# Kernel tuning notes

Hardware: AMD Instinct MI355X
Metric: run time of the kernel (lower is better)

Reference implementation:

```python
import jax, jax.numpy as jnp
import numpy as np

LAMBDA_GEO = 0.5


def setup_inputs() -> dict:
    key = jax.random.key(0)
    embeddings = jax.random.normal(key, (4, 2048, 512), dtype=jnp.float32)
    return {"embeddings": embeddings}


def _geometric_loss(embeddings):
    b, s, d = embeddings.shape
    x = embeddings.reshape(b * s, d)  # [N, d]
    sq_norm = jnp.sum(x * x, axis=-1)  # [N]
    sq = sq_norm[:, None] + sq_norm[None, :] - 2.0 * (x @ x.T)  # [N, N]
    sq = jnp.maximum(sq, 0.0)
    dist = jnp.sqrt(sq)  # torch.cdist(p=2)
    return jnp.mean(jnp.exp(-dist * 0.1)) * 0.1


def reference(embeddings):
    geometric_loss = _geometric_loss(embeddings)
    total_geometric = LAMBDA_GEO * geometric_loss
    return geometric_loss, total_geometric
```

## Files before the change

kernel.cpp:

```cpp
#include <hip/hip_runtime.h>

#define NROWS 8192
#define DIM   512
#define NT    64
#define NTRI  (NT * (NT + 1) / 2)
#define NACC  64

typedef __attribute__((ext_vector_type(16))) float f32x16;
typedef __attribute__((ext_vector_type(8)))  int   i32x8;

__device__ __forceinline__ unsigned char f2e4m3(float x) {
    unsigned ux = __float_as_uint(x);
    unsigned s  = (ux >> 24) & 0x80u;
    float a = __uint_as_float(ux & 0x7FFFFFFFu);
    a = fminf(a, 448.0f);
    unsigned ua = __float_as_uint(a);
    int eb = (int)(ua >> 23);
    if (eb < 121) eb = 121;
    float step  = __uint_as_float((unsigned)(eb - 3) << 23);
    float istep = __uint_as_float((unsigned)(257 - eb) << 23);
    float q = rintf(a * istep) * step;
    q = fminf(q, 448.0f);
    if (q < 0.001953125f)
        return (unsigned char)s;
    unsigned uq = __float_as_uint(q);
    int eq = (int)(uq >> 23) - 127;
    unsigned byte;
    if (eq < -6) byte = (unsigned)(q * 512.0f);
    else         byte = (unsigned)((eq + 7) << 3) | ((uq >> 20) & 7u);
    return (unsigned char)(s | byte);
}

__global__ __launch_bounds__(256) void norm_convert_kernel(
    const float* __restrict__ X, unsigned char* __restrict__ Xq,
    float* __restrict__ norms, float* __restrict__ acc)
{
    const int tid  = threadIdx.x;
    const int lane = tid & 63;
    const int w    = tid >> 6;
    const int row  = blockIdx.x * 4 + w;

    if (blockIdx.x == 0 && tid < NACC + 1) acc[tid] = 0.0f;

    const float* xr = X + (size_t)row * DIM + lane * 8;
    float4 v0 = *(const float4*)xr;
    float4 v1 = *(const float4*)(xr + 4);

    float s = 0.0f;
    s = fmaf(v0.x, v0.x, s); s = fmaf(v0.y, v0.y, s);
    s = fmaf(v0.z, v0.z, s); s = fmaf(v0.w, v0.w, s);
    s = fmaf(v1.x, v1.x, s); s = fmaf(v1.y, v1.y, s);
    s = fmaf(v1.z, v1.z, s); s = fmaf(v1.w, v1.w, s);

    union { unsigned char b[8]; uint2 v; } pk;
    pk.b[0] = f2e4m3(v0.x); pk.b[1] = f2e4m3(v0.y);
    pk.b[2] = f2e4m3(v0.z); pk.b[3] = f2e4m3(v0.w);
    pk.b[4] = f2e4m3(v1.x); pk.b[5] = f2e4m3(v1.y);
    pk.b[6] = f2e4m3(v1.z); pk.b[7] = f2e4m3(v1.w);

    const int slab = lane >> 3;
    const int c16  = (lane >> 1) & 3;
    const int cpos = c16 ^ ((row >> 1) & 3);
    *(uint2*)(Xq + (size_t)row * DIM + slab * 64 + cpos * 16 + (lane & 1) * 8)
        = pk.v;

    #pragma unroll
    for (int off = 32; off > 0; off >>= 1) s += __shfl_down(s, off, 64);
    if (lane == 0) norms[row] = s;
}

__device__ __forceinline__ void gload16(const void* g, void* l) {
    __builtin_amdgcn_global_load_lds(
        (const __attribute__((address_space(1))) unsigned int*)g,
        (__attribute__((address_space(3))) unsigned int*)l, 16, 0, 0);
}

__global__ __launch_bounds__(256, 3) void pair_loss_gemm_kernel(
    const unsigned char* __restrict__ Xq, const float* __restrict__ norms,
    float* __restrict__ acc, float* __restrict__ out)
{
    __shared__ __align__(16) char Ls[3][16384];
    __shared__ float wsum[4];
    __shared__ int lastflag;

    const int bid = (blockIdx.x & 7) * 260 + (blockIdx.x >> 3);
    int t = bid, bi = 0;
    while (t >= (NT - bi)) { t -= (NT - bi); bi++; }
    const int bj = bi + t;

    const int tid  = threadIdx.x;
    const int lane = tid & 63;
    const int w    = tid >> 6;

    const int rowA = bi * 128;
    const int rowB = bj * 128;

    f32x16 accv[2][2];
    #pragma unroll
    for (int a = 0; a < 2; a++)
        #pragma unroll
        for (int b = 0; b < 2; b++)
            #pragma unroll
            for (int r = 0; r < 16; r++) accv[a][b][r] = 0.0f;

    const int lrow = lane >> 2;
    const int lpos = ((lane & 3) ^ ((lane >> 3) & 3)) * 16;
    const unsigned char* gA0 = Xq + (size_t)(rowA + w * 32 + lrow) * DIM + lpos;
    const unsigned char* gA1 = gA0 + (size_t)16 * DIM;
    const unsigned char* gB0 = Xq + (size_t)(rowB + w * 32 + lrow) * DIM + lpos;
    const unsigned char* gB1 = gB0 + (size_t)16 * DIM;
    const int dst0 = (w * 32) * 64;
    const int dst1 = (w * 32 + 16) * 64;

    const int rl = lane & 31;
    const int qh = lane >> 5;
    const int p0 = ((2 * qh) ^ ((rl >> 1) & 3)) * 16;
    const int p1 = p0 ^ 16;
    const int wr = (w & 1) * 64;
    const int wc = (w >> 1) * 64;
    const int ra = (wr + rl) * 64;
    const int rb = 8192 + (wc + rl) * 64;

#define STAGE(s) do {                                                    \
        char* sl_ = Ls[(s) % 3];                                         \
        const int kb_ = (s) * 64;                                        \
        gload16(gA0 + kb_, sl_ + dst0);                                  \
        gload16(gA1 + kb_, sl_ + dst1);                                  \
        gload16(gB0 + kb_, sl_ + 8192 + dst0);                           \
        gload16(gB1 + kb_, sl_ + 8192 + dst1);                           \
    } while (0)

    STAGE(0);
    STAGE(1);

    #pragma unroll
    for (int k = 0; k < 8; k++) {
        __builtin_amdgcn_sched_barrier(0);
        if (k < 7) asm volatile("s_waitcnt vmcnt(4)" ::: "memory");
        else       asm volatile("s_waitcnt vmcnt(0)" ::: "memory");
        __builtin_amdgcn_s_barrier();
        __builtin_amdgcn_sched_barrier(0);

        if (k < 6) STAGE(k + 2);

        const char* sl = Ls[k % 3];
        union frag { uint4 u[2]; i32x8 v; };
        frag fa0, fa1, fb0, fb1;
        fa0.u[0] = *(const uint4*)(sl + ra + p0);
        fa0.u[1] = *(const uint4*)(sl + ra + p1);
        fa1.u[0] = *(const uint4*)(sl + ra + 2048 + p0);
        fa1.u[1] = *(const uint4*)(sl + ra + 2048 + p1);
        fb0.u[0] = *(const uint4*)(sl + rb + p0);
        fb0.u[1] = *(const uint4*)(sl + rb + p1);
        fb1.u[0] = *(const uint4*)(sl + rb + 2048 + p0);
        fb1.u[1] = *(const uint4*)(sl + rb + 2048 + p1);

        __builtin_amdgcn_s_setprio(1);
        accv[0][0] = __builtin_amdgcn_mfma_scale_f32_32x32x64_f8f6f4(
            fa0.v, fb0.v, accv[0][0], 0, 0, 0, 0x7F7F7F7F, 0, 0x7F7F7F7F);
        accv[0][1] = __builtin_amdgcn_mfma_scale_f32_32x32x64_f8f6f4(
            fa0.v, fb1.v, accv[0][1], 0, 0, 0, 0x7F7F7F7F, 0, 0x7F7F7F7F);
        accv[1][0] = __builtin_amdgcn_mfma_scale_f32_32x32x64_f8f6f4(
            fa1.v, fb0.v, accv[1][0], 0, 0, 0, 0x7F7F7F7F, 0, 0x7F7F7F7F);
        accv[1][1] = __builtin_amdgcn_mfma_scale_f32_32x32x64_f8f6f4(
            fa1.v, fb1.v, accv[1][1], 0, 0, 0, 0x7F7F7F7F, 0, 0x7F7F7F7F);
        __builtin_amdgcn_s_setprio(0);
        __builtin_amdgcn_sched_barrier(0);
    }
#undef STAGE

    const float wgt = (bi == bj) ? 1.0f : 2.0f;
    const int cl = lane & 31;
    const int rh = qh * 4;
    float lsum = 0.0f;
    #pragma unroll
    for (int a = 0; a < 2; a++) {
        const int gia = rowA + wr + a * 32;
        float ni[16];
        #pragma unroll
        for (int r = 0; r < 16; r++)
            ni[r] = norms[gia + (r & 3) + 8 * (r >> 2) + rh];
        #pragma unroll
        for (int b = 0; b < 2; b++) {
            const int gj = rowB + wc + b * 32 + cl;
            const float nj = norms[gj];
            #pragma unroll
            for (int r = 0; r < 4; r++) {
            }
            #pragma unroll
            for (int r = 0; r < 16; r++) {
                const int gi = gia + (r & 3) + 8 * (r >> 2) + rh;
                float sq = fmaf(-2.0f, accv[a][b][r], ni[r] + nj);
                sq = fmaxf(sq, 0.0f);
                float term = __expf(-0.1f * sqrtf(sq));
                if (gi == gj) term = 1.0f;
                lsum += term;
            }
        }
    }
    lsum *= wgt;
    #pragma unroll
    for (int off = 32; off > 0; off >>= 1) lsum += __shfl_down(lsum, off, 64);
    if (lane == 0) wsum[w] = lsum;
    __syncthreads();

    if (tid == 0) {
        float bsum = wsum[0] + wsum[1] + wsum[2] + wsum[3];
        float old = atomicAdd(&acc[bid & (NACC - 1)], bsum);
        asm volatile("" :: "v"(old));
        unsigned prev = atomicAdd((unsigned int*)(acc + NACC), 1u);
        lastflag = (prev == NTRI - 1) ? 1 : 0;
    }
    __syncthreads();
    if (lastflag && tid < 64) {
        float v = atomicAdd(&acc[tid], 0.0f);
        #pragma unroll
        for (int off = 32; off > 0; off >>= 1) v += __shfl_down(v, off, 64);
        if (tid == 0) {
            const float inv = 1.0f / ((float)NROWS * (float)NROWS);
            float loss = v * inv * 0.1f;
            out[0] = loss;
            out[1] = 0.5f * loss;
        }
    }
}

extern "C" void kernel_launch(void* const* d_in, const int* in_sizes, int n_in,
                              void* d_out, int out_size, void* d_ws, size_t ws_size,
                              hipStream_t stream)
{
    const float* X = (const float*)d_in[0];
    float* out = (float*)d_out;

    char* ws = (char*)d_ws;
    float*         acc   = (float*)ws;
    float*         norms = (float*)(ws + 1024);
    unsigned char* Xq    = (unsigned char*)(ws + 1024 + 32768);

    norm_convert_kernel<<<NROWS / 4, 256, 0, stream>>>(X, Xq, norms, acc);
    pair_loss_gemm_kernel<<<NTRI, 256, 0, stream>>>(Xq, norms, acc, out);
}
```

Measured before the change: 109.5 us.

## Use K-slab fp8 layout and direct global fragment loads, dropping LDS staging

After: 129.6 us. 1.18x slower.

```diff
diff --git a/kernel.cpp b/kernel.cpp
--- a/kernel.cpp
+++ b/kernel.cpp
@@ -2,8 +2,9 @@
 
 #define NROWS 8192
 #define DIM   512
-#define NT    64
-#define NTRI  (NT * (NT + 1) / 2)
+#define KSLAB (NROWS * 64)
+#define NPAIR 528
+#define NBLK  (NPAIR * 4)
 #define NACC  64
 
 typedef __attribute__((ext_vector_type(16))) float f32x16;
@@ -58,42 +59,39 @@
     pk.b[4] = f2e4m3(v1.x); pk.b[5] = f2e4m3(v1.y);
     pk.b[6] = f2e4m3(v1.z); pk.b[7] = f2e4m3(v1.w);
 
-    const int slab = lane >> 3;
-    const int c16  = (lane >> 1) & 3;
-    const int cpos = c16 ^ ((row >> 1) & 3);
-    *(uint2*)(Xq + (size_t)row * DIM + slab * 64 + cpos * 16 + (lane & 1) * 8)
-        = pk.v;
+    *(uint2*)(Xq + (size_t)(lane >> 3) * KSLAB + (size_t)row * 64
+              + (lane & 7) * 8) = pk.v;
 
     #pragma unroll
     for (int off = 32; off > 0; off >>= 1) s += __shfl_down(s, off, 64);
     if (lane == 0) norms[row] = s;
-}
-
-__device__ __forceinline__ void gload16(const void* g, void* l) {
-    __builtin_amdgcn_global_load_lds(
-        (const __attribute__((address_space(1))) unsigned int*)g,
-        (__attribute__((address_space(3))) unsigned int*)l, 16, 0, 0);
 }
 
 __global__ __launch_bounds__(256, 3) void pair_loss_gemm_kernel(
     const unsigned char* __restrict__ Xq, const float* __restrict__ norms,
     float* __restrict__ acc, float* __restrict__ out)
 {
-    __shared__ __align__(16) char Ls[3][16384];
     __shared__ float wsum[4];
     __shared__ int lastflag;
 
-    const int bid = (blockIdx.x & 7) * 260 + (blockIdx.x >> 3);
-    int t = bid, bi = 0;
-    while (t >= (NT - bi)) { t -= (NT - bi); bi++; }
-    const int bj = bi + t;
+    const int bid = (blockIdx.x & 7) * 264 + (blockIdx.x >> 3);
+    int t = bid >> 2, G = 0;
+    while (t >= (32 - G)) { t -= (32 - G); G++; }
+    const int g = G + t;
 
     const int tid  = threadIdx.x;
     const int lane = tid & 63;
     const int w    = tid >> 6;
 
-    const int rowA = bi * 128;
-    const int rowB = bj * 128;
+    const int bi = 4 * G + (bid & 3);
+    const int bj = 4 * g + w;
+    const int rowA = bi * 64;
+    const int rowB = bj * 64;
+
+    const int rl = lane & 31;
+    const int qh = lane >> 5;
+    const unsigned char* pA = Xq + (size_t)(rowA + rl) * 64 + qh * 32;
+    const unsigned char* pB = Xq + (size_t)(rowB + rl) * 64 + qh * 32;
 
     f32x16 accv[2][2];
     #pragma unroll
@@ -103,90 +101,67 @@
             #pragma unroll
             for (int r = 0; r < 16; r++) accv[a][b][r] = 0.0f;
 
-    const int lrow = lane >> 2;
-    const int lpos = ((lane & 3) ^ ((lane >> 3) & 3)) * 16;
-    const unsigned char* gA0 = Xq + (size_t)(rowA + w * 32 + lrow) * DIM + lpos;
-    const unsigned char* gA1 = gA0 + (size_t)16 * DIM;
-    const unsigned char* gB0 = Xq + (size_t)(rowB + w * 32 + lrow) * DIM + lpos;
-    const unsigned char* gB1 = gB0 + (size_t)16 * DIM;
-    const int dst0 = (w * 32) * 64;
-    const int dst1 = (w * 32 + 16) * 64;
-
-    const int rl = lane & 31;
-    const int qh = lane >> 5;
-    const int p0 = ((2 * qh) ^ ((rl >> 1) & 3)) * 16;
-    const int p1 = p0 ^ 16;
-    const int wr = (w & 1) * 64;
-    const int wc = (w >> 1) * 64;
-    const int ra = (wr + rl) * 64;
-    const int rb = 8192 + (wc + rl) * 64;
-
-#define STAGE(s) do {                                                    \
-        char* sl_ = Ls[(s) % 3];                                         \
-        const int kb_ = (s) * 64;                                        \
-        gload16(gA0 + kb_, sl_ + dst0);                                  \
-        gload16(gA1 + kb_, sl_ + dst1);                                  \
-        gload16(gB0 + kb_, sl_ + 8192 + dst0);                           \
-        gload16(gB1 + kb_, sl_ + 8192 + dst1);                           \
+    union frag { uint4 u[2]; i32x8 v; };
+
+#define LOADF(dst, base, off) do {                                       \
+        (dst).u[0] = *(const uint4*)((base) + (off));                    \
+        (dst).u[1] = *(const uint4*)((base) + (off) + 16);               \
     } while (0)
 
-    STAGE(0);
-    STAGE(1);
-
-    #pragma unroll
-    for (int k = 0; k < 8; k++) {
-        __builtin_amdgcn_sched_barrier(0);
-        if (k < 7) asm volatile("s_waitcnt vmcnt(4)" ::: "memory");
-        else       asm volatile("s_waitcnt vmcnt(0)" ::: "memory");
-        __builtin_amdgcn_s_barrier();
-        __builtin_amdgcn_sched_barrier(0);
-
-        if (k < 6) STAGE(k + 2);
-
-        const char* sl = Ls[k % 3];
-        union frag { uint4 u[2]; i32x8 v; };
-        frag fa0, fa1, fb0, fb1;
-        fa0.u[0] = *(const uint4*)(sl + ra + p0);
-        fa0.u[1] = *(const uint4*)(sl + ra + p1);
-        fa1.u[0] = *(const uint4*)(sl + ra + 2048 + p0);
-        fa1.u[1] = *(const uint4*)(sl + ra + 2048 + p1);
-        fb0.u[0] = *(const uint4*)(sl + rb + p0);
-        fb0.u[1] = *(const uint4*)(sl + rb + p1);
-        fb1.u[0] = *(const uint4*)(sl + rb + 2048 + p0);
-        fb1.u[1] = *(const uint4*)(sl + rb + 2048 + p1);
-
-        __builtin_amdgcn_s_setprio(1);
-        accv[0][0] = __builtin_amdgcn_mfma_scale_f32_32x32x64_f8f6f4(
-            fa0.v, fb0.v, accv[0][0], 0, 0, 0, 0x7F7F7F7F, 0, 0x7F7F7F7F);
-        accv[0][1] = __builtin_amdgcn_mfma_scale_f32_32x32x64_f8f6f4(
-            fa0.v, fb1.v, accv[0][1], 0, 0, 0, 0x7F7F7F7F, 0, 0x7F7F7F7F);
-        accv[1][0] = __builtin_amdgcn_mfma_scale_f32_32x32x64_f8f6f4(
-            fa1.v, fb0.v, accv[1][0], 0, 0, 0, 0x7F7F7F7F, 0, 0x7F7F7F7F);
-        accv[1][1] = __builtin_amdgcn_mfma_scale_f32_32x32x64_f8f6f4(
-            fa1.v, fb1.v, accv[1][1], 0, 0, 0, 0x7F7F7F7F, 0, 0x7F7F7F7F);
-        __builtin_amdgcn_s_setprio(0);
-        __builtin_amdgcn_sched_barrier(0);
-    }
-#undef STAGE
-
-    const float wgt = (bi == bj) ? 1.0f : 2.0f;
+#define MFMA4(A0, A1, B0, B1) do {                                       \
+        accv[0][0] = __builtin_amdgcn_mfma_scale_f32_32x32x64_f8f6f4(    \
+            (A0).v, (B0).v, accv[0][0], 0, 0, 0, 0x7F7F7F7F, 0, 0x7F7F7F7F); \
+        accv[0][1] = __builtin_amdgcn_mfma_scale_f32_32x32x64_f8f6f4(    \
+            (A0).v, (B1).v, accv[0][1], 0, 0, 0, 0x7F7F7F7F, 0, 0x7F7F7F7F); \
+        accv[1][0] = __builtin_amdgcn_mfma_scale_f32_32x32x64_f8f6f4(    \
+            (A1).v, (B0).v, accv[1][0], 0, 0, 0, 0x7F7F7F7F, 0, 0x7F7F7F7F); \
+        accv[1][1] = __builtin_amdgcn_mfma_scale_f32_32x32x64_f8f6f4(    \
+            (A1).v, (B1).v, accv[1][1], 0, 0, 0, 0x7F7F7F7F, 0, 0x7F7F7F7F); \
+    } while (0)
+
+    frag a0e, a1e, b0e, b1e;
+    frag a0o, a1o, b0o, b1o;
+    LOADF(a0e, pA, (size_t)0);
+    LOADF(a1e, pA, (size_t)2048);
+    LOADF(b0e, pB, (size_t)0);
+    LOADF(b1e, pB, (size_t)2048);
+
+    #pragma unroll
+    for (int kk = 0; kk < 4; kk++) {
+        const size_t k1 = (size_t)(2 * kk + 1) * KSLAB;
+        LOADF(a0o, pA, k1);
+        LOADF(a1o, pA, k1 + 2048);
+        LOADF(b0o, pB, k1);
+        LOADF(b1o, pB, k1 + 2048);
+        MFMA4(a0e, a1e, b0e, b1e);
+
+        if (kk < 3) {
+            const size_t k2 = (size_t)(2 * kk + 2) * KSLAB;
+            LOADF(a0e, pA, k2);
+            LOADF(a1e, pA, k2 + 2048);
+            LOADF(b0e, pB, k2);
+            LOADF(b1e, pB, k2 + 2048);
+        }
+        MFMA4(a0o, a1o, b0o, b1o);
+    }
+#undef MFMA4
+#undef LOADF
+
+    const float wgt = (bj < bi) ? 0.0f : ((bj == bi) ? 1.0f : 2.0f);
     const int cl = lane & 31;
     const int rh = qh * 4;
     float lsum = 0.0f;
     #pragma unroll
     for (int a = 0; a < 2; a++) {
-        const int gia = rowA + wr + a * 32;
+        const int gia = rowA + a * 32;
         float ni[16];
         #pragma unroll
         for (int r = 0; r < 16; r++)
             ni[r] = norms[gia + (r & 3) + 8 * (r >> 2) + rh];
         #pragma unroll
         for (int b = 0; b < 2; b++) {
-            const int gj = rowB + wc + b * 32 + cl;
+            const int gj = rowB + b * 32 + cl;
             const float nj = norms[gj];
-            #pragma unroll
-            for (int r = 0; r < 4; r++) {
-            }
             #pragma unroll
             for (int r = 0; r < 16; r++) {
                 const int gi = gia + (r & 3) + 8 * (r >> 2) + rh;
@@ -209,7 +184,7 @@
         float old = atomicAdd(&acc[bid & (NACC - 1)], bsum);
         asm volatile("" :: "v"(old));
         unsigned prev = atomicAdd((unsigned int*)(acc + NACC), 1u);
-        lastflag = (prev == NTRI - 1) ? 1 : 0;
+        lastflag = (prev == NBLK - 1) ? 1 : 0;
     }
     __syncthreads();
     if (lastflag && tid < 64) {
@@ -238,5 +213,5 @@
     unsigned char* Xq    = (unsigned char*)(ws + 1024 + 32768);
 
     norm_convert_kernel<<<NROWS / 4, 256, 0, stream>>>(X, Xq, norms, acc);
-    pair_loss_gemm_kernel<<<NTRI, 256, 0, stream>>>(Xq, norms, acc, out);
-}
+    pair_loss_gemm_kernel<<<NBLK, 256, 0, stream>>>(Xq, norms, acc, out);
+}
```
